# Kernel optimization log

Hardware: AMD Instinct MI355X
Metric: run time of the kernel (lower is better)

## Reference

```python
import jax, jax.numpy as jnp
import numpy as np

B, NQ, NKV, D, H = 2, 2048, 2048, 1024, 16
DH = D // H
EPS = 1e-5


def _ln(x, g, b):
    mu = jnp.mean(x, axis=-1, keepdims=True)
    var = jnp.mean(jnp.square(x - mu), axis=-1, keepdims=True)
    return (x - mu) * jax.lax.rsqrt(var + EPS) * g + b


def setup_inputs() -> dict:
    key = jax.random.key(0)
    ks = jax.random.split(key, 16)
    s = 0.02
    return {
        "X": jax.random.normal(ks[0], (B, NQ, D), jnp.float32),
        "Y": jax.random.normal(ks[1], (B, NKV, D), jnp.float32),
        "Wq": jax.random.normal(ks[2], (D, D), jnp.float32) * s,
        "bq": jnp.zeros((D,), jnp.float32),
        "Wk": jax.random.normal(ks[3], (D, D), jnp.float32) * s,
        "bk": jnp.zeros((D,), jnp.float32),
        "Wv": jax.random.normal(ks[4], (D, D), jnp.float32) * s,
        "bv": jnp.zeros((D,), jnp.float32),
        "null_k": jax.random.normal(ks[5], (1, 1, D), jnp.float32) * s,
        "g0": jnp.ones((D,), jnp.float32),
        "b0": jnp.zeros((D,), jnp.float32),
        "g0kv": jnp.ones((D,), jnp.float32),
        "b0kv": jnp.zeros((D,), jnp.float32),
        "g1": jnp.ones((D,), jnp.float32),
        "b1": jnp.zeros((D,), jnp.float32),
        "W1": jax.random.normal(ks[6], (D, 4 * D), jnp.float32) * s,
        "bf1": jnp.zeros((4 * D,), jnp.float32),
        "W2": jax.random.normal(ks[7], (4 * D, D), jnp.float32) * s,
        "bf2": jnp.zeros((D,), jnp.float32),
    }


def reference(X, Y, Wq, bq, Wk, bk, Wv, bv, null_k, g0, b0, g0kv, b0kv,
              g1, b1, W1, bf1, W2, bf2):
    # pre-layer-norm on Q-side and KV-side inputs
    Xn = _ln(X, g0, b0)
    Yn = _ln(Y, g0kv, b0kv)
    Q = Xn @ Wq + bq                       # [B, NQ, D]
    K = Yn @ Wk + bk                       # [B, NKV, D]
    V = Yn @ Wv + bv
    # null KV: learned null key, zero value appended along seq dim
    K = jnp.concatenate([K, jnp.broadcast_to(null_k, (B, 1, D))], axis=1)   # [B, NKV+1, D]
    V = jnp.concatenate([V, jnp.zeros((B, 1, D), V.dtype)], axis=1)
    # split heads (split along feature dim == reshape to (.., H, DH))
    Qh = Q.reshape(B, NQ, H, DH)
    Kh = K.reshape(B, NKV + 1, H, DH)
    Vh = V.reshape(B, NKV + 1, H, DH)
    # scores scaled by 1/sqrt(dim_KV) (NOT head dim), softmax_temp == 1.0
    A = jnp.einsum('bqhd,bkhd->bhqk', Qh, Kh) / jnp.sqrt(jnp.float32(D))
    A = jax.nn.softmax(A, axis=-1)          # [B, H, NQ, NKV+1]
    O = jnp.einsum('bhqk,bkhd->bqhd', A, Vh).reshape(B, NQ, D)
    # no head mixing (fc_mix_heads=None); residual uses identity fc_res
    Hres = O + X
    Hr = _ln(Hres, g1, b1)
    ff = jax.nn.gelu(Hr @ W1 + bf1, approximate=False) @ W2 + bf2
    return Hres + ff
```

## Files before the change

kernel.cpp:

```cpp
#include <hip/hip_runtime.h>
#include <hip/hip_bf16.h>
#include <math.h>
#include <stdint.h>

typedef __bf16 bf16x8 __attribute__((ext_vector_type(8)));
typedef __bf16 bf16x4 __attribute__((ext_vector_type(4)));
typedef float floatx4 __attribute__((ext_vector_type(4)));
typedef short shortx4 __attribute__((ext_vector_type(4)));

#define NQS   2048
#define NKVS  2048
#define NKV1  2049
#define DM    1024
#define NH    16
#define DHD   64
#define BATCH 2
#define ROWS  (BATCH * NQS)

__device__ __forceinline__ void gld_lds16(const __bf16* gp, __bf16* lp) {
    __builtin_amdgcn_global_load_lds(
        (const __attribute__((address_space(1))) uint32_t*)(uintptr_t)gp,
        (__attribute__((address_space(3))) uint32_t*)(uintptr_t)lp,
        16, 0, 0);
}

__device__ __forceinline__ float gelu_fast(float x) {
    const float u = x * x;
    const float e = __builtin_amdgcn_exp2f(x * (-2.3022077f + (-0.1029431f) * u));
    return x * __builtin_amdgcn_rcpf(1.0f + e);
}

__global__ __launch_bounds__(256) void ln2_to_bf16(
    const float* __restrict__ X, const float* __restrict__ Y,
    const float* __restrict__ g0, const float* __restrict__ b0,
    const float* __restrict__ g0kv, const float* __restrict__ b0kv,
    __bf16* __restrict__ Xn, __bf16* __restrict__ Yn)
{
    int row = blockIdx.x;
    const float *src, *gamma, *beta; __bf16* dst;
    if (row < ROWS) { src = X; gamma = g0; beta = b0; dst = Xn; }
    else { row -= ROWS; src = Y; gamma = g0kv; beta = b0kv; dst = Yn; }
    const int tid = threadIdx.x;
    const float4 v = ((const float4*)(src + (size_t)row * DM))[tid];
    float s  = v.x + v.y + v.z + v.w;
    float sq = v.x * v.x + v.y * v.y + v.z * v.z + v.w * v.w;
    for (int off = 1; off < 64; off <<= 1) {
        s  += __shfl_xor(s, off);
        sq += __shfl_xor(sq, off);
    }
    __shared__ float red[8];
    const int wave = tid >> 6, lane = tid & 63;
    if (lane == 0) { red[wave * 2] = s; red[wave * 2 + 1] = sq; }
    __syncthreads();
    s  = red[0] + red[2] + red[4] + red[6];
    sq = red[1] + red[3] + red[5] + red[7];
    const float mu  = s * (1.0f / DM);
    const float var = sq * (1.0f / DM) - mu * mu;
    const float rs  = rsqrtf(var + 1e-5f);
    const float4 gv = ((const float4*)gamma)[tid];
    const float4 bv = ((const float4*)beta)[tid];
    bf16x4 o;
    o[0] = (__bf16)((v.x - mu) * rs * gv.x + bv.x);
    o[1] = (__bf16)((v.y - mu) * rs * gv.y + bv.y);
    o[2] = (__bf16)((v.z - mu) * rs * gv.z + bv.z);
    o[3] = (__bf16)((v.w - mu) * rs * gv.w + bv.w);
    *(bf16x4*)(dst + (size_t)row * DM + tid * 4) = o;
}

__global__ __launch_bounds__(256) void resid_ln(
    const float* __restrict__ X, const __bf16* __restrict__ O,
    const float* __restrict__ gamma, const float* __restrict__ beta,
    float* __restrict__ Hres, __bf16* __restrict__ Hr)
{
    const int row = blockIdx.x;
    const int tid = threadIdx.x;
    const float4 xv = ((const float4*)(X + (size_t)row * DM))[tid];
    const bf16x4 ov = *(const bf16x4*)(O + (size_t)row * DM + tid * 4);
    float4 v;
    v.x = xv.x + (float)ov[0];
    v.y = xv.y + (float)ov[1];
    v.z = xv.z + (float)ov[2];
    v.w = xv.w + (float)ov[3];
    ((float4*)(Hres + (size_t)row * DM))[tid] = v;

    float s  = v.x + v.y + v.z + v.w;
    float sq = v.x * v.x + v.y * v.y + v.z * v.z + v.w * v.w;
    for (int off = 1; off < 64; off <<= 1) {
        s  += __shfl_xor(s, off);
        sq += __shfl_xor(sq, off);
    }
    __shared__ float red[8];
    const int wave = tid >> 6, lane = tid & 63;
    if (lane == 0) { red[wave * 2] = s; red[wave * 2 + 1] = sq; }
    __syncthreads();
    s  = red[0] + red[2] + red[4] + red[6];
    sq = red[1] + red[3] + red[5] + red[7];
    const float mu  = s * (1.0f / DM);
    const float var = sq * (1.0f / DM) - mu * mu;
    const float rs  = rsqrtf(var + 1e-5f);
    const float4 gv = ((const float4*)gamma)[tid];
    const float4 bv = ((const float4*)beta)[tid];
    bf16x4 o;
    o[0] = (__bf16)((v.x - mu) * rs * gv.x + bv.x);
    o[1] = (__bf16)((v.y - mu) * rs * gv.y + bv.y);
    o[2] = (__bf16)((v.z - mu) * rs * gv.z + bv.z);
    o[3] = (__bf16)((v.w - mu) * rs * gv.w + bv.w);
    *(bf16x4*)(Hr + (size_t)row * DM + tid * 4) = o;
}

__global__ __launch_bounds__(256) void transpose3_f32_bf16(
    const float* __restrict__ Wq, const float* __restrict__ Wk,
    const float* __restrict__ Wv, __bf16* __restrict__ WqT,
    __bf16* __restrict__ WkT, __bf16* __restrict__ WvT)
{
    __shared__ float tile[32][33];
    const int z = blockIdx.z;
    const float* in = (z == 0) ? Wq : (z == 1) ? Wk : Wv;
    __bf16* out = (z == 0) ? WqT : (z == 1) ? WkT : WvT;
    const int c0 = blockIdx.x * 32, r0 = blockIdx.y * 32;
    const int tx = threadIdx.x, ty = threadIdx.y;
#pragma unroll
    for (int i = 0; i < 4; i++)
        tile[ty + i * 8][tx] = in[(size_t)(r0 + ty + i * 8) * DM + c0 + tx];
    __syncthreads();
#pragma unroll
    for (int i = 0; i < 4; i++)
        out[(size_t)(c0 + ty + i * 8) * DM + r0 + tx] = (__bf16)tile[tx][ty + i * 8];
}

__global__ __launch_bounds__(256) void transpose_ffw(
    const float* __restrict__ W1, const float* __restrict__ W2,
    __bf16* __restrict__ W1T, __bf16* __restrict__ W2T)
{
    __shared__ float tile[32][33];
    const int z = blockIdx.z;
    const float* in; __bf16* out; int R, C, c0, r0;
    if (z == 0) { in = W1; out = W1T; R = DM; C = 4 * DM; c0 = blockIdx.x * 32; r0 = blockIdx.y * 32; }
    else        { in = W2; out = W2T; R = 4 * DM; C = DM; c0 = blockIdx.y * 32; r0 = blockIdx.x * 32; }
    const int tx = threadIdx.x, ty = threadIdx.y;
#pragma unroll
    for (int i = 0; i < 4; i++)
        tile[ty + i * 8][tx] = in[(size_t)(r0 + ty + i * 8) * C + c0 + tx];
    __syncthreads();
#pragma unroll
    for (int i = 0; i < 4; i++)
        out[(size_t)(c0 + ty + i * 8) * R + r0 + tx] = (__bf16)tile[tx][ty + i * 8];
}

__global__ __launch_bounds__(256) void fill_null(
    const float* __restrict__ null_k, __bf16* __restrict__ Kb,
    __bf16* __restrict__ Vt)
{
    const int i = blockIdx.x * 256 + threadIdx.x;
    if (i < BATCH * DM) {
        const int b = i >> 10, d = i & (DM - 1);
        Kb[((size_t)b * NKV1 + NKVS) * DM + d] = (__bf16)null_k[d];
    }
    if (i < BATCH * NH * DHD * 8) {
        const int bhd = i >> 3, kvp = i & 7;
        Vt[(size_t)bhd * 2056 + 2048 + kvp] = (__bf16)0.0f;
    }
}

__device__ __forceinline__ void g256_loop(
    const __bf16* __restrict__ A, const __bf16* __restrict__ Bt,
    int Kst, int kbeg, int m0, int n0,
    __bf16* sa, __bf16* sb, floatx4 (&acc)[8][4])
{
    const int tid = threadIdx.x, lane = tid & 63;
    const int g = lane >> 4, c = lane & 15;
    const int wave = tid >> 6;
    const int wm = wave >> 2, wn = wave & 3;

    const int r = tid >> 2, j = tid & 3;
    const int jx = (j ^ (r & 3)) * 8;
    const __bf16* Ag = A  + (size_t)(m0 + r) * Kst + kbeg + jx;
    const __bf16* Bg = Bt + (size_t)(n0 + r) * Kst + kbeg + jx;
    __bf16* la = sa + tid * 8;
    __bf16* lb = sb + tid * 8;

#define G256_STAGE(ss, koff) do {                                          \
    gld_lds16(Ag + (koff),                      la + (ss) * 8192);         \
    gld_lds16(Ag + (size_t)128 * Kst + (koff),  la + (ss) * 8192 + 4096);  \
    gld_lds16(Bg + (koff),                      lb + (ss) * 8192);         \
    gld_lds16(Bg + (size_t)128 * Kst + (koff),  lb + (ss) * 8192 + 4096);  \
} while (0)

    G256_STAGE(0, 0);
    G256_STAGE(1, 32);
    G256_STAGE(2, 64);

    const int ca = (c & 3) * 8;
    const __bf16* ra = sa + (wm * 128 + c) * 32;
    const __bf16* rb = sb + (wn * 64 + c) * 32;

    for (int s = 0; s < 32; s++) {
        if (s < 29) {
            G256_STAGE((s + 3) & 3, (s + 3) * 32);
            asm volatile("s_waitcnt vmcnt(12)" ::: "memory");
        } else if (s == 29) {
            asm volatile("s_waitcnt vmcnt(8)" ::: "memory");
        } else if (s == 30) {
            asm volatile("s_waitcnt vmcnt(4)" ::: "memory");
        } else {
            asm volatile("s_waitcnt vmcnt(0)" ::: "memory");
        }
        __builtin_amdgcn_sched_barrier(0);
        __builtin_amdgcn_s_barrier();
        asm volatile("" ::: "memory");

        const int ss = (s & 3) * 8192;
        bf16x8 af[8], bfr[4];
#pragma unroll
        for (int i = 0; i < 8; i++)
            af[i] = *(const bf16x8*)(ra + ss + i * 512 + ((g * 8) ^ ca));
#pragma unroll
        for (int jj = 0; jj < 4; jj++)
            bfr[jj] = *(const bf16x8*)(rb + ss + jj * 512 + ((g * 8) ^ ca));

        __builtin_amdgcn_s_setprio(1);
#pragma unroll
        for (int i = 0; i < 8; i++)
#pragma unroll
            for (int jj = 0; jj < 4; jj++)
                acc[i][jj] = __builtin_amdgcn_mfma_f32_16x16x32_bf16(
                    af[i], bfr[jj], acc[i][jj], 0, 0, 0);
        __builtin_amdgcn_s_setprio(0);
        __builtin_amdgcn_sched_barrier(0);
        __builtin_amdgcn_s_barrier();
        asm volatile("" ::: "memory");
    }
#undef G256_STAGE
}

template<int NX>
__device__ __forceinline__ void g256_decode(int bid, int ntot, int& m0, int& n0)
{
    const int cpx = ntot >> 3;
    const int l = (bid & 7) * cpx + (bid >> 3);
    m0 = (l / NX) * 256;
    n0 = (l % NX) * 256;
}

template<int MODE, int ACT, int NX>
__global__ __launch_bounds__(512, 2) void g256(
    const __bf16* __restrict__ A, const __bf16* __restrict__ Bt,
    const float* __restrict__ bias, void* __restrict__ outp,
    int M, int N, int Kst)
{
    __shared__ __bf16 SA[4][256][32];
    __shared__ __bf16 SB[4][256][32];
    int m0, n0;
    g256_decode<NX>(blockIdx.x, NX * (M >> 8), m0, n0);
    const int kbeg = (MODE == 4) ? (blockIdx.z << 10) : 0;

    floatx4 acc[8][4] = {};
    g256_loop(A, Bt, Kst, kbeg, m0, n0, &SA[0][0][0], &SB[0][0][0], acc);

    const int tid = threadIdx.x, lane = tid & 63, wave = tid >> 6;
    const int g = lane >> 4, c = lane & 15;
    const int wm = wave >> 2, wn = wave & 3;

    __bf16* obf = (__bf16*)outp;
    float*  of  = (float*)outp;
#pragma unroll
    for (int i = 0; i < 8; i++) {
#pragma unroll
        for (int jj = 0; jj < 4; jj++) {
            const int row = m0 + wm * 128 + i * 16 + g * 4;
            const int col = n0 + wn * 64 + jj * 16 + c;
            const float bb = (MODE == 4) ? 0.0f : bias[col];
            float xs[4];
#pragma unroll
            for (int rr = 0; rr < 4; rr++) {
                float x = acc[i][jj][rr] + bb;
                if (ACT == 1) x = gelu_fast(x);
                xs[rr] = x;
            }
            if (MODE == 0) {
#pragma unroll
                for (int rr = 0; rr < 4; rr++)
                    obf[(size_t)(row + rr) * N + col] = (__bf16)xs[rr];
            } else if (MODE == 4) {
#pragma unroll
                for (int rr = 0; rr < 4; rr++)
                    of[((size_t)blockIdx.z * M + row + rr) * N + col] = xs[rr];
            }
        }
    }
}

__global__ __launch_bounds__(512, 2) void g256qkv(
    const __bf16* __restrict__ Xn, const __bf16* __restrict__ Yn,
    const __bf16* __restrict__ WqT, const __bf16* __restrict__ WkT,
    const __bf16* __restrict__ WvT,
    const float* __restrict__ bq, const float* __restrict__ bk,
    const float* __restrict__ bv,
    __bf16* __restrict__ Qbf, __bf16* __restrict__ Kbf,
    __bf16* __restrict__ Vt)
{
    __shared__ __bf16 SA[4][256][32];
    __shared__ __bf16 SB[4][256][32];
    const int z = blockIdx.z;
    const __bf16* A    = (z == 0) ? Xn  : Yn;
    const __bf16* Bt   = (z == 0) ? WqT : (z == 1) ? WkT : WvT;
    const float*  bias = (z == 0) ? bq  : (z == 1) ? bk  : bv;

    int m0, n0;
    g256_decode<4>(blockIdx.x, 64, m0, n0);

    floatx4 acc[8][4] = {};
    g256_loop(A, Bt, DM, 0, m0, n0, &SA[0][0][0], &SB[0][0][0], acc);

    const int tid = threadIdx.x, lane = tid & 63, wave = tid >> 6;
    const int g = lane >> 4, c = lane & 15;
    const int wm = wave >> 2, wn = wave & 3;

#pragma unroll
    for (int i = 0; i < 8; i++) {
#pragma unroll
        for (int jj = 0; jj < 4; jj++) {
            const int row = m0 + wm * 128 + i * 16 + g * 4;
            const int col = n0 + wn * 64 + jj * 16 + c;
            const float bb = bias[col];
            float xs[4];
#pragma unroll
            for (int rr = 0; rr < 4; rr++) xs[rr] = acc[i][jj][rr] + bb;
            if (z == 0) {
#pragma unroll
                for (int rr = 0; rr < 4; rr++)
                    Qbf[(size_t)(row + rr) * DM + col] = (__bf16)xs[rr];
            } else if (z == 1) {
#pragma unroll
                for (int rr = 0; rr < 4; rr++) {
                    const int r2 = row + rr;
                    Kbf[(size_t)(r2 + (r2 >> 11)) * DM + col] = (__bf16)xs[rr];
                }
            } else {
                const int b  = row >> 11;
                const int kv = row & 2047;
                const size_t base =
                    ((size_t)((b * NH + (col >> 6)) * DHD + (col & 63))) * 2056 + kv;
                bf16x4 pk;
                pk[0] = (__bf16)xs[0]; pk[1] = (__bf16)xs[1];
                pk[2] = (__bf16)xs[2]; pk[3] = (__bf16)xs[3];
                *(bf16x4*)(Vt + base) = pk;
            }
        }
    }
}

__global__ __launch_bounds__(256) void ff2_reduce(
    const float* __restrict__ part, const float* __restrict__ bias,
    const float* __restrict__ Hres, float* __restrict__ out)
{
    const size_t f4 = (size_t)blockIdx.x * 256 + threadIdx.x;
    const int c4 = (int)(f4 & (DM / 4 - 1));
    const size_t stride4 = (size_t)ROWS * DM / 4;
    float4 a = ((const float4*)part)[f4];
    const float4 p1 = ((const float4*)part)[f4 + stride4];
    const float4 p2 = ((const float4*)part)[f4 + 2 * stride4];
    const float4 p3 = ((const float4*)part)[f4 + 3 * stride4];
    const float4 b  = ((const float4*)bias)[c4];
    const float4 hr = ((const float4*)Hres)[f4];
    a.x += p1.x + p2.x + p3.x + b.x + hr.x;
    a.y += p1.y + p2.y + p3.y + b.y + hr.y;
    a.z += p1.z + p2.z + p3.z + b.z + hr.z;
    a.w += p1.w + p2.w + p3.w + b.w + hr.w;
    ((float4*)out)[f4] = a;
}

__global__ __launch_bounds__(256, 2) void attn_kernel(
    const __bf16* __restrict__ Q, const __bf16* __restrict__ Kb,
    const __bf16* __restrict__ Vt, __bf16* __restrict__ O)
{
    __shared__ __bf16 Ks[4][64][64];
    __shared__ __bf16 Vs[4][64][64];

    const int tid = threadIdx.x, lane = tid & 63, w = tid >> 6;
    const int g = lane >> 4, c = lane & 15;

    const int hw   = blockIdx.x;
    const int slot = hw >> 3;
    const int hb   = (hw & 7) | ((slot >> 4) << 3);
    const int h = hb & 15, b = hb >> 4;
    const int q0w = (slot & 15) * 128 + w * 32;

    const float QSC = 0.03125f * 1.44269504088896f;
    bf16x8 qf[2][2];
#pragma unroll
    for (int qt = 0; qt < 2; qt++) {
        const __bf16* Qbase = Q + ((size_t)(b * NQS + q0w + qt * 16 + c)) * DM + h * DHD;
        qf[qt][0] = *(const bf16x8*)(Qbase + g * 8);
        qf[qt][1] = *(const bf16x8*)(Qbase + 32 + g * 8);
#pragma unroll
        for (int e = 0; e < 8; e++) {
            qf[qt][0][e] = (__bf16)((float)qf[qt][0][e] * QSC);
            qf[qt][1][e] = (__bf16)((float)qf[qt][1][e] * QSC);
        }
    }

    shortx4 ones;
    ones[0] = ones[1] = ones[2] = ones[3] = (short)0x3F80;

    floatx4 dacc[2] = {};
    floatx4 oacc[2][4] = {};

    const int srow = tid >> 3;
    const int schk = (tid & 7) ^ (srow & 7);
    const __bf16* Kg  = Kb + (size_t)b * NKV1 * DM + h * DHD + schk * 8;
    const __bf16* Vg  = Vt + ((size_t)(b * NH + h) * DHD + srow) * 2056;
    const __bf16* Vg2 = Vg + (size_t)32 * 2056;
    const int vcol0 = schk * 8;

    auto stage = [&](int p, int kv0, bool tail) {
        __bf16* kd0 = &Ks[p][0][0]  + tid * 8;
        __bf16* kd1 = &Ks[p][32][0] + tid * 8;
        __bf16* vd0 = &Vs[p][0][0]  + tid * 8;
        __bf16* vd1 = &Vs[p][32][0] + tid * 8;
        if (!tail) {
            gld_lds16(Kg + (size_t)(kv0 + srow) * DM, kd0);
            gld_lds16(Kg + (size_t)(kv0 + srow + 32) * DM, kd1);
            gld_lds16(Vg + kv0 + vcol0, vd0);
            gld_lds16(Vg2 + kv0 + vcol0, vd1);
        } else {
            const int r0 = min(kv0 + srow, NKVS);
            const int r1 = min(kv0 + srow + 32, NKVS);
            const int vc = min(kv0 + vcol0, NKVS);
            gld_lds16(Kg + (size_t)r0 * DM, kd0);
            gld_lds16(Kg + (size_t)r1 * DM, kd1);
            gld_lds16(Vg + vc, vd0);
            gld_lds16(Vg2 + vc, vd1);
        }
    };

    auto compute = [&](int p, int kv0, bool tail) {
        floatx4 s[2][4];
#pragma unroll
        for (int qt = 0; qt < 2; qt++)
#pragma unroll
            for (int kvt = 0; kvt < 4; kvt++)
#pragma unroll
                for (int r = 0; r < 4; r++) s[qt][kvt][r] = -6.0f;

        const int sw = c & 7;
        __builtin_amdgcn_s_setprio(1);
#pragma unroll
        for (int kvt = 0; kvt < 4; kvt++) {
            const bf16x8 kf0 = *(const bf16x8*)&Ks[p][kvt * 16 + c][(g ^ sw) * 8];
            const bf16x8 kf1 = *(const bf16x8*)&Ks[p][kvt * 16 + c][((4 | g) ^ sw) * 8];
#pragma unroll
            for (int qt = 0; qt < 2; qt++) {
                s[qt][kvt] = __builtin_amdgcn_mfma_f32_16x16x32_bf16(kf0, qf[qt][0], s[qt][kvt], 0, 0, 0);
                s[qt][kvt] = __builtin_amdgcn_mfma_f32_16x16x32_bf16(kf1, qf[qt][1], s[qt][kvt], 0, 0, 0);
            }
        }
        __builtin_amdgcn_s_setprio(0);

        if (tail) {
#pragma unroll
            for (int qt = 0; qt < 2; qt++)
#pragma unroll
                for (int kvt = 0; kvt < 4; kvt++)
#pragma unroll
                    for (int r = 0; r < 4; r++)
                        if (kv0 + kvt * 16 + g * 4 + r >= NKV1) s[qt][kvt][r] = -1e30f;
        }

        shortx4 pf[2][4];
#pragma unroll
        for (int qt = 0; qt < 2; qt++)
#pragma unroll
            for (int kvt = 0; kvt < 4; kvt++) {
                const unsigned u0 = __builtin_bit_cast(unsigned, __builtin_amdgcn_exp2f(s[qt][kvt][0]));
                const unsigned u1 = __builtin_bit_cast(unsigned, __builtin_amdgcn_exp2f(s[qt][kvt][1]));
                const unsigned u2 = __builtin_bit_cast(unsigned, __builtin_amdgcn_exp2f(s[qt][kvt][2]));
                const unsigned u3 = __builtin_bit_cast(unsigned, __builtin_amdgcn_exp2f(s[qt][kvt][3]));
                unsigned pk0 = __builtin_amdgcn_perm(u1, u0, 0x07060302u);
                unsigned pk1 = __builtin_amdgcn_perm(u3, u2, 0x07060302u);
                unsigned long long pk = ((unsigned long long)pk1 << 32) | pk0;
                pf[qt][kvt] = __builtin_bit_cast(shortx4, pk);
            }

        __builtin_amdgcn_s_setprio(1);
#pragma unroll
        for (int kvt = 0; kvt < 4; kvt++) {
            shortx4 vfr[4];
#pragma unroll
            for (int dt = 0; dt < 4; dt++) {
                const int slotp = (kvt * 2 + (g >> 1)) ^ sw;
                vfr[dt] = *(const shortx4*)&Vs[p][dt * 16 + c][slotp * 8 + (g & 1) * 4];
            }
#pragma unroll
            for (int dt = 0; dt < 4; dt++)
#pragma unroll
                for (int qt = 0; qt < 2; qt++)
                    oacc[qt][dt] = __builtin_amdgcn_mfma_f32_16x16x16bf16_1k(
                        vfr[dt], pf[qt][kvt], oacc[qt][dt], 0, 0, 0);
#pragma unroll
            for (int qt = 0; qt < 2; qt++)
                dacc[qt] = __builtin_amdgcn_mfma_f32_16x16x16bf16_1k(
                    ones, pf[qt][kvt], dacc[qt], 0, 0, 0);
        }
        __builtin_amdgcn_s_setprio(0);
    };

    stage(0, 0, false);
    stage(1, 64, false);
    __syncthreads();
    for (int it = 0; it < 32; it += 2) {
        stage((it + 2) & 3, (it + 2) * 64, (it + 2) == 32);
        if (it + 3 <= 32) stage((it + 3) & 3, (it + 3) * 64, false);
        compute(it & 3, it * 64, false);
        compute((it + 1) & 3, (it + 1) * 64, false);
        __syncthreads();
    }
    compute(0, 2048, true);

#pragma unroll
    for (int qt = 0; qt < 2; qt++) {
        const float inv_l = 1.0f / dacc[qt][0];
        __bf16* Ob = O + ((size_t)(b * NQS + q0w + qt * 16 + c)) * DM + h * DHD;
#pragma unroll
        for (int dt = 0; dt < 4; dt++) {
            bf16x4 ob;
#pragma unroll
            for (int r = 0; r < 4; r++) ob[r] = (__bf16)(oacc[qt][dt][r] * inv_l);
            *(bf16x4*)(Ob + dt * 16 + g * 4) = ob;
        }
    }
}

extern "C" void kernel_launch(void* const* d_in, const int* in_sizes, int n_in,
                              void* d_out, int out_size, void* d_ws, size_t ws_size,
                              hipStream_t stream)
{
    const float* X      = (const float*)d_in[0];
    const float* Y      = (const float*)d_in[1];
    const float* Wq     = (const float*)d_in[2];
    const float* bq     = (const float*)d_in[3];
    const float* Wk     = (const float*)d_in[4];
    const float* bk     = (const float*)d_in[5];
    const float* Wv     = (const float*)d_in[6];
    const float* bv     = (const float*)d_in[7];
    const float* null_k = (const float*)d_in[8];
    const float* g0     = (const float*)d_in[9];
    const float* b0     = (const float*)d_in[10];
    const float* g0kv   = (const float*)d_in[11];
    const float* b0kv   = (const float*)d_in[12];
    const float* g1     = (const float*)d_in[13];
    const float* b1     = (const float*)d_in[14];
    const float* W1     = (const float*)d_in[15];
    const float* bf1    = (const float*)d_in[16];
    const float* W2     = (const float*)d_in[17];
    const float* bf2    = (const float*)d_in[18];
    float* out = (float*)d_out;

    char* p = (char*)d_ws;
    __bf16* W2T  = (__bf16*)p; p += (size_t)4 * DM * DM * 2;
    float*  Hres = (float*)p;  p += (size_t)ROWS * DM * 4;
    __bf16* Gbf  = (__bf16*)p; p += (size_t)ROWS * 4 * DM * 2;
    char* scratch = p;
    __bf16* Xn   = (__bf16*)p; p += (size_t)ROWS * DM * 2;
    __bf16* Yn   = (__bf16*)p; p += (size_t)ROWS * DM * 2;
    __bf16* WqT  = (__bf16*)p; p += (size_t)DM * DM * 2;
    __bf16* WkT  = (__bf16*)p; p += (size_t)DM * DM * 2;
    __bf16* WvT  = (__bf16*)p; p += (size_t)DM * DM * 2;
    __bf16* W1T  = (__bf16*)p; p += (size_t)4 * DM * DM * 2;
    __bf16* Qbf  = (__bf16*)p; p += (size_t)ROWS * DM * 2;
    __bf16* Kbf  = (__bf16*)p; p += (size_t)BATCH * NKV1 * DM * 2;
    __bf16* Vt   = (__bf16*)p; p += (size_t)BATCH * NH * DHD * 2056 * 2;
    __bf16* Obf  = (__bf16*)p; p += (size_t)ROWS * DM * 2;
    __bf16* Hr   = (__bf16*)p; p += (size_t)ROWS * DM * 2;
    float* Part  = (float*)scratch;

    ln2_to_bf16<<<2 * ROWS, 256, 0, stream>>>(X, Y, g0, b0, g0kv, b0kv, Xn, Yn);

    transpose3_f32_bf16<<<dim3(DM / 32, DM / 32, 3), dim3(32, 8), 0, stream>>>(
        Wq, Wk, Wv, WqT, WkT, WvT);
    transpose_ffw<<<dim3(128, 32, 2), dim3(32, 8), 0, stream>>>(W1, W2, W1T, W2T);

    g256qkv<<<dim3(64, 1, 3), 512, 0, stream>>>(
        Xn, Yn, WqT, WkT, WvT, bq, bk, bv, Qbf, Kbf, Vt);
    fill_null<<<64, 256, 0, stream>>>(null_k, Kbf, Vt);

    attn_kernel<<<dim3(512), 256, 0, stream>>>(Qbf, Kbf, Vt, Obf);

    resid_ln<<<ROWS, 256, 0, stream>>>(X, Obf, g1, b1, Hres, Hr);

    g256<0, 1, 16><<<dim3(256), 512, 0, stream>>>(
        Hr, W1T, bf1, (void*)Gbf, ROWS, 4 * DM, DM);
    g256<4, 0, 4><<<dim3(64, 1, 4), 512, 0, stream>>>(
        Gbf, W2T, bf2, (void*)Part, ROWS, DM, 4 * DM);
    ff2_reduce<<<ROWS * DM / 1024, 256, 0, stream>>>(Part, bf2, Hres, out);
}
```

Before: 353.0 us.

## Interleave LDS reads, global prefetch and MFMA in four phases per k-step

Restructures the 256x256 GEMM main loop so each k-step is split into four phases. Each phase loads two A fragments from LDS, issues one of the four global-to-LDS prefetch loads, synchronizes, and runs eight MFMAs. The vmcnt wait is relaxed to match the spread-out issue. The intent is to overlap LDS reads and global loads with MFMA work and lower register pressure by holding only two A fragments at a time. It also lowers launch bounds from two to one block per CU, which frees registers but may cut occupancy, and adds three extra barriers per k-step.

```diff
diff --git a/kernel.cpp b/kernel.cpp
--- a/kernel.cpp
+++ b/kernel.cpp
@@ -193,42 +193,89 @@
     const int ca = (c & 3) * 8;
     const __bf16* ra = sa + (wm * 128 + c) * 32;
     const __bf16* rb = sb + (wn * 64 + c) * 32;
+    const int rx = (g * 8) ^ ca;
 
     for (int s = 0; s < 32; s++) {
-        if (s < 29) {
-            G256_STAGE((s + 3) & 3, (s + 3) * 32);
-            asm volatile("s_waitcnt vmcnt(12)" ::: "memory");
-        } else if (s == 29) {
-            asm volatile("s_waitcnt vmcnt(8)" ::: "memory");
-        } else if (s == 30) {
-            asm volatile("s_waitcnt vmcnt(4)" ::: "memory");
-        } else {
-            asm volatile("s_waitcnt vmcnt(0)" ::: "memory");
-        }
+        if (s <= 29)      asm volatile("s_waitcnt vmcnt(8)" ::: "memory");
+        else if (s == 30) asm volatile("s_waitcnt vmcnt(4)" ::: "memory");
+        else              asm volatile("s_waitcnt vmcnt(0)" ::: "memory");
         __builtin_amdgcn_sched_barrier(0);
         __builtin_amdgcn_s_barrier();
         asm volatile("" ::: "memory");
 
         const int ss = (s & 3) * 8192;
-        bf16x8 af[8], bfr[4];
-#pragma unroll
-        for (int i = 0; i < 8; i++)
-            af[i] = *(const bf16x8*)(ra + ss + i * 512 + ((g * 8) ^ ca));
-#pragma unroll
-        for (int jj = 0; jj < 4; jj++)
-            bfr[jj] = *(const bf16x8*)(rb + ss + jj * 512 + ((g * 8) ^ ca));
-
+        const bool st = (s < 29);
+        const int s3 = (s + 3) & 3;
+        const int k3 = (s + 3) * 32;
+        bf16x8 bfr[4], a0, a1;
+
+        bfr[0] = *(const bf16x8*)(rb + ss + 0 * 512 + rx);
+        bfr[1] = *(const bf16x8*)(rb + ss + 1 * 512 + rx);
+        bfr[2] = *(const bf16x8*)(rb + ss + 2 * 512 + rx);
+        bfr[3] = *(const bf16x8*)(rb + ss + 3 * 512 + rx);
+        a0 = *(const bf16x8*)(ra + ss + 0 * 512 + rx);
+        a1 = *(const bf16x8*)(ra + ss + 1 * 512 + rx);
+        if (st) gld_lds16(Ag + k3, la + s3 * 8192);
+        __builtin_amdgcn_sched_barrier(0);
+        __builtin_amdgcn_s_barrier();
+        asm volatile("s_waitcnt lgkmcnt(0)" ::: "memory");
+        __builtin_amdgcn_sched_barrier(0);
         __builtin_amdgcn_s_setprio(1);
 #pragma unroll
-        for (int i = 0; i < 8; i++)
-#pragma unroll
-            for (int jj = 0; jj < 4; jj++)
-                acc[i][jj] = __builtin_amdgcn_mfma_f32_16x16x32_bf16(
-                    af[i], bfr[jj], acc[i][jj], 0, 0, 0);
+        for (int jj = 0; jj < 4; jj++) {
+            acc[0][jj] = __builtin_amdgcn_mfma_f32_16x16x32_bf16(a0, bfr[jj], acc[0][jj], 0, 0, 0);
+            acc[1][jj] = __builtin_amdgcn_mfma_f32_16x16x32_bf16(a1, bfr[jj], acc[1][jj], 0, 0, 0);
+        }
         __builtin_amdgcn_s_setprio(0);
         __builtin_amdgcn_sched_barrier(0);
+
+        a0 = *(const bf16x8*)(ra + ss + 2 * 512 + rx);
+        a1 = *(const bf16x8*)(ra + ss + 3 * 512 + rx);
+        if (st) gld_lds16(Ag + (size_t)128 * Kst + k3, la + s3 * 8192 + 4096);
+        __builtin_amdgcn_sched_barrier(0);
         __builtin_amdgcn_s_barrier();
-        asm volatile("" ::: "memory");
+        asm volatile("s_waitcnt lgkmcnt(0)" ::: "memory");
+        __builtin_amdgcn_sched_barrier(0);
+        __builtin_amdgcn_s_setprio(1);
+#pragma unroll
+        for (int jj = 0; jj < 4; jj++) {
+            acc[2][jj] = __builtin_amdgcn_mfma_f32_16x16x32_bf16(a0, bfr[jj], acc[2][jj], 0, 0, 0);
+            acc[3][jj] = __builtin_amdgcn_mfma_f32_16x16x32_bf16(a1, bfr[jj], acc[3][jj], 0, 0, 0);
+        }
+        __builtin_amdgcn_s_setprio(0);
+        __builtin_amdgcn_sched_barrier(0);
+
+        a0 = *(const bf16x8*)(ra + ss + 4 * 512 + rx);
+        a1 = *(const bf16x8*)(ra + ss + 5 * 512 + rx);
+        if (st) gld_lds16(Bg + k3, lb + s3 * 8192);
+        __builtin_amdgcn_sched_barrier(0);
+        __builtin_amdgcn_s_barrier();
+        asm volatile("s_waitcnt lgkmcnt(0)" ::: "memory");
+        __builtin_amdgcn_sched_barrier(0);
+        __builtin_amdgcn_s_setprio(1);
+#pragma unroll
+        for (int jj = 0; jj < 4; jj++) {
+            acc[4][jj] = __builtin_amdgcn_mfma_f32_16x16x32_bf16(a0, bfr[jj], acc[4][jj], 0, 0, 0);
+            acc[5][jj] = __builtin_amdgcn_mfma_f32_16x16x32_bf16(a1, bfr[jj], acc[5][jj], 0, 0, 0);
+        }
+        __builtin_amdgcn_s_setprio(0);
+        __builtin_amdgcn_sched_barrier(0);
+
+        a0 = *(const bf16x8*)(ra + ss + 6 * 512 + rx);
+        a1 = *(const bf16x8*)(ra + ss + 7 * 512 + rx);
+        if (st) gld_lds16(Bg + (size_t)128 * Kst + k3, lb + s3 * 8192 + 4096);
+        __builtin_amdgcn_sched_barrier(0);
+        __builtin_amdgcn_s_barrier();
+        asm volatile("s_waitcnt lgkmcnt(0)" ::: "memory");
+        __builtin_amdgcn_sched_barrier(0);
+        __builtin_amdgcn_s_setprio(1);
+#pragma unroll
+        for (int jj = 0; jj < 4; jj++) {
+            acc[6][jj] = __builtin_amdgcn_mfma_f32_16x16x32_bf16(a0, bfr[jj], acc[6][jj], 0, 0, 0);
+            acc[7][jj] = __builtin_amdgcn_mfma_f32_16x16x32_bf16(a1, bfr[jj], acc[7][jj], 0, 0, 0);
+        }
+        __builtin_amdgcn_s_setprio(0);
+        __builtin_amdgcn_sched_barrier(0);
     }
 #undef G256_STAGE
 }
@@ -243,7 +290,7 @@
 }
 
 template<int MODE, int ACT, int NX>
-__global__ __launch_bounds__(512, 2) void g256(
+__global__ __launch_bounds__(512, 1) void g256(
     const __bf16* __restrict__ A, const __bf16* __restrict__ Bt,
     const float* __restrict__ bias, void* __restrict__ outp,
     int M, int N, int Kst)
@@ -290,7 +337,7 @@
     }
 }
 
-__global__ __launch_bounds__(512, 2) void g256qkv(
+__global__ __launch_bounds__(512, 1) void g256qkv(
     const __bf16* __restrict__ Xn, const __bf16* __restrict__ Yn,
     const __bf16* __restrict__ WqT, const __bf16* __restrict__ WkT,
     const __bf16* __restrict__ WvT,
```

Result: faster. 342.0 us (-3.1%).

## Shrink GEMM tiles to 128x128 with 256-thread blocks and double buffering

Applied to the files above, without the earlier changes.

Replaces the 256x256 GEMM tile (512 threads, 4-stage LDS pipeline) with a 128x128 tile (256 threads, 2-stage pipeline) for the QKV, FF1 and FF2 GEMMs. Grid sizes grow four-fold, which gives the 256 CUs more blocks and better load balance, and lets more blocks fit per CU. In exchange each tile reuses its loaded data less, so global traffic per FLOP goes up, and the shallower prefetch exposes more memory latency.

```diff
diff --git a/kernel.cpp b/kernel.cpp
--- a/kernel.cpp
+++ b/kernel.cpp
@@ -162,15 +162,15 @@
     }
 }
 
-__device__ __forceinline__ void g256_loop(
+__device__ __forceinline__ void g128_loop(
     const __bf16* __restrict__ A, const __bf16* __restrict__ Bt,
-    int Kst, int kbeg, int m0, int n0,
-    __bf16* sa, __bf16* sb, floatx4 (&acc)[8][4])
+    int Kst, int kbeg, int ns, int m0, int n0,
+    __bf16* sa, __bf16* sb, floatx4 (&acc)[4][4])
 {
     const int tid = threadIdx.x, lane = tid & 63;
     const int g = lane >> 4, c = lane & 15;
     const int wave = tid >> 6;
-    const int wm = wave >> 2, wn = wave & 3;
+    const int wm = (wave >> 1) * 64, wn = (wave & 1) * 64;
 
     const int r = tid >> 2, j = tid & 3;
     const int jx = (j ^ (r & 3)) * 8;
@@ -179,28 +179,22 @@
     __bf16* la = sa + tid * 8;
     __bf16* lb = sb + tid * 8;
 
-#define G256_STAGE(ss, koff) do {                                          \
-    gld_lds16(Ag + (koff),                      la + (ss) * 8192);         \
-    gld_lds16(Ag + (size_t)128 * Kst + (koff),  la + (ss) * 8192 + 4096);  \
-    gld_lds16(Bg + (koff),                      lb + (ss) * 8192);         \
-    gld_lds16(Bg + (size_t)128 * Kst + (koff),  lb + (ss) * 8192 + 4096);  \
+#define G128_STAGE(ss, koff) do {                                         \
+    gld_lds16(Ag + (koff),                     la + (ss) * 4096);         \
+    gld_lds16(Ag + (size_t)64 * Kst + (koff),  la + (ss) * 4096 + 2048);  \
+    gld_lds16(Bg + (koff),                     lb + (ss) * 4096);         \
+    gld_lds16(Bg + (size_t)64 * Kst + (koff),  lb + (ss) * 4096 + 2048);  \
 } while (0)
 
-    G256_STAGE(0, 0);
-    G256_STAGE(1, 32);
-    G256_STAGE(2, 64);
-
-    const int ca = (c & 3) * 8;
-    const __bf16* ra = sa + (wm * 128 + c) * 32;
-    const __bf16* rb = sb + (wn * 64 + c) * 32;
-
-    for (int s = 0; s < 32; s++) {
-        if (s < 29) {
-            G256_STAGE((s + 3) & 3, (s + 3) * 32);
-            asm volatile("s_waitcnt vmcnt(12)" ::: "memory");
-        } else if (s == 29) {
-            asm volatile("s_waitcnt vmcnt(8)" ::: "memory");
-        } else if (s == 30) {
+    G128_STAGE(0, 0);
+
+    const int rx = (g * 8) ^ ((c & 3) * 8);
+    const __bf16* ra = sa + (wm + c) * 32;
+    const __bf16* rb = sb + (wn + c) * 32;
+
+    for (int s = 0; s < ns; s++) {
+        if (s + 1 < ns) {
+            G128_STAGE((s + 1) & 1, (s + 1) * 32);
             asm volatile("s_waitcnt vmcnt(4)" ::: "memory");
         } else {
             asm volatile("s_waitcnt vmcnt(0)" ::: "memory");
@@ -209,18 +203,18 @@
         __builtin_amdgcn_s_barrier();
         asm volatile("" ::: "memory");
 
-        const int ss = (s & 3) * 8192;
-        bf16x8 af[8], bfr[4];
-#pragma unroll
-        for (int i = 0; i < 8; i++)
-            af[i] = *(const bf16x8*)(ra + ss + i * 512 + ((g * 8) ^ ca));
+        const int ss = (s & 1) * 4096;
+        bf16x8 af[4], bfr[4];
+#pragma unroll
+        for (int i = 0; i < 4; i++)
+            af[i] = *(const bf16x8*)(ra + ss + i * 512 + rx);
 #pragma unroll
         for (int jj = 0; jj < 4; jj++)
-            bfr[jj] = *(const bf16x8*)(rb + ss + jj * 512 + ((g * 8) ^ ca));
+            bfr[jj] = *(const bf16x8*)(rb + ss + jj * 512 + rx);
 
         __builtin_amdgcn_s_setprio(1);
 #pragma unroll
-        for (int i = 0; i < 8; i++)
+        for (int i = 0; i < 4; i++)
 #pragma unroll
             for (int jj = 0; jj < 4; jj++)
                 acc[i][jj] = __builtin_amdgcn_mfma_f32_16x16x32_bf16(
@@ -230,45 +224,46 @@
         __builtin_amdgcn_s_barrier();
         asm volatile("" ::: "memory");
     }
-#undef G256_STAGE
+#undef G128_STAGE
 }
 
 template<int NX>
-__device__ __forceinline__ void g256_decode(int bid, int ntot, int& m0, int& n0)
+__device__ __forceinline__ void g128_decode(int bid, int ntot, int& m0, int& n0)
 {
     const int cpx = ntot >> 3;
     const int l = (bid & 7) * cpx + (bid >> 3);
-    m0 = (l / NX) * 256;
-    n0 = (l % NX) * 256;
+    m0 = (l / NX) * 128;
+    n0 = (l % NX) * 128;
 }
 
 template<int MODE, int ACT, int NX>
-__global__ __launch_bounds__(512, 2) void g256(
+__global__ __launch_bounds__(256, 4) void g128(
     const __bf16* __restrict__ A, const __bf16* __restrict__ Bt,
     const float* __restrict__ bias, void* __restrict__ outp,
-    int M, int N, int Kst)
-{
-    __shared__ __bf16 SA[4][256][32];
-    __shared__ __bf16 SB[4][256][32];
+    int M, int N, int K)
+{
+    __shared__ __bf16 SA[2][128][32];
+    __shared__ __bf16 SB[2][128][32];
     int m0, n0;
-    g256_decode<NX>(blockIdx.x, NX * (M >> 8), m0, n0);
-    const int kbeg = (MODE == 4) ? (blockIdx.z << 10) : 0;
-
-    floatx4 acc[8][4] = {};
-    g256_loop(A, Bt, Kst, kbeg, m0, n0, &SA[0][0][0], &SB[0][0][0], acc);
+    g128_decode<NX>(blockIdx.x, NX * (M >> 7), m0, n0);
+    const int kbeg = (MODE == 4) ? blockIdx.z * (K >> 2) : 0;
+    const int ns = ((MODE == 4) ? (K >> 2) : K) >> 5;
+
+    floatx4 acc[4][4] = {};
+    g128_loop(A, Bt, K, kbeg, ns, m0, n0, &SA[0][0][0], &SB[0][0][0], acc);
 
     const int tid = threadIdx.x, lane = tid & 63, wave = tid >> 6;
     const int g = lane >> 4, c = lane & 15;
-    const int wm = wave >> 2, wn = wave & 3;
+    const int wm = (wave >> 1) * 64, wn = (wave & 1) * 64;
 
     __bf16* obf = (__bf16*)outp;
     float*  of  = (float*)outp;
 #pragma unroll
-    for (int i = 0; i < 8; i++) {
+    for (int i = 0; i < 4; i++) {
 #pragma unroll
         for (int jj = 0; jj < 4; jj++) {
-            const int row = m0 + wm * 128 + i * 16 + g * 4;
-            const int col = n0 + wn * 64 + jj * 16 + c;
+            const int row = m0 + wm + i * 16 + g * 4;
+            const int col = n0 + wn + jj * 16 + c;
             const float bb = (MODE == 4) ? 0.0f : bias[col];
             float xs[4];
 #pragma unroll
@@ -290,7 +285,7 @@
     }
 }
 
-__global__ __launch_bounds__(512, 2) void g256qkv(
+__global__ __launch_bounds__(256, 4) void g128qkv(
     const __bf16* __restrict__ Xn, const __bf16* __restrict__ Yn,
     const __bf16* __restrict__ WqT, const __bf16* __restrict__ WkT,
     const __bf16* __restrict__ WvT,
@@ -299,29 +294,29 @@
     __bf16* __restrict__ Qbf, __bf16* __restrict__ Kbf,
     __bf16* __restrict__ Vt)
 {
-    __shared__ __bf16 SA[4][256][32];
-    __shared__ __bf16 SB[4][256][32];
+    __shared__ __bf16 SA[2][128][32];
+    __shared__ __bf16 SB[2][128][32];
     const int z = blockIdx.z;
     const __bf16* A    = (z == 0) ? Xn  : Yn;
     const __bf16* Bt   = (z == 0) ? WqT : (z == 1) ? WkT : WvT;
     const float*  bias = (z == 0) ? bq  : (z == 1) ? bk  : bv;
 
     int m0, n0;
-    g256_decode<4>(blockIdx.x, 64, m0, n0);
-
-    floatx4 acc[8][4] = {};
-    g256_loop(A, Bt, DM, 0, m0, n0, &SA[0][0][0], &SB[0][0][0], acc);
+    g128_decode<8>(blockIdx.x, 256, m0, n0);
+
+    floatx4 acc[4][4] = {};
+    g128_loop(A, Bt, DM, 0, DM >> 5, m0, n0, &SA[0][0][0], &SB[0][0][0], acc);
 
     const int tid = threadIdx.x, lane = tid & 63, wave = tid >> 6;
     const int g = lane >> 4, c = lane & 15;
-    const int wm = wave >> 2, wn = wave & 3;
-
-#pragma unroll
-    for (int i = 0; i < 8; i++) {
+    const int wm = (wave >> 1) * 64, wn = (wave & 1) * 64;
+
+#pragma unroll
+    for (int i = 0; i < 4; i++) {
 #pragma unroll
         for (int jj = 0; jj < 4; jj++) {
-            const int row = m0 + wm * 128 + i * 16 + g * 4;
-            const int col = n0 + wn * 64 + jj * 16 + c;
+            const int row = m0 + wm + i * 16 + g * 4;
+            const int col = n0 + wn + jj * 16 + c;
             const float bb = bias[col];
             float xs[4];
 #pragma unroll
@@ -580,7 +575,7 @@
         Wq, Wk, Wv, WqT, WkT, WvT);
     transpose_ffw<<<dim3(128, 32, 2), dim3(32, 8), 0, stream>>>(W1, W2, W1T, W2T);
 
-    g256qkv<<<dim3(64, 1, 3), 512, 0, stream>>>(
+    g128qkv<<<dim3(256, 1, 3), 256, 0, stream>>>(
         Xn, Yn, WqT, WkT, WvT, bq, bk, bv, Qbf, Kbf, Vt);
     fill_null<<<64, 256, 0, stream>>>(null_k, Kbf, Vt);
 
@@ -588,9 +583,9 @@
 
     resid_ln<<<ROWS, 256, 0, stream>>>(X, Obf, g1, b1, Hres, Hr);
 
-    g256<0, 1, 16><<<dim3(256), 512, 0, stream>>>(
+    g128<0, 1, 32><<<1024, 256, 0, stream>>>(
         Hr, W1T, bf1, (void*)Gbf, ROWS, 4 * DM, DM);
-    g256<4, 0, 4><<<dim3(64, 1, 4), 512, 0, stream>>>(
+    g128<4, 0, 8><<<dim3(256, 1, 4), 256, 0, stream>>>(
         Gbf, W2T, bf2, (void*)Part, ROWS, DM, 4 * DM);
     ff2_reduce<<<ROWS * DM / 1024, 256, 0, stream>>>(Part, bf2, Hres, out);
 }
```

Result: no change. 353.6 us (+0.2%).

## Restructure 256x256 GEMM mainloop to double-buffered K=64 tiles with interleaved loads

Applied to the files above, without the earlier changes.

The GEMM mainloop switches from a 4-stage K=32 LDS ring to a 2-stage K=64 double buffer. The next tile's global-to-LDS loads are split across four compute sub-phases so they overlap with MFMA work. A new XOR swizzle is used for the wider rows. LDS grows to 128KB per block, so launch bounds drop to one block per CU. The aim is fewer barriers per K and better load/compute interleaving, at the cost of occupancy and extra intra-tile barriers.

```diff
diff --git a/kernel.cpp b/kernel.cpp
--- a/kernel.cpp
+++ b/kernel.cpp
@@ -164,7 +164,7 @@
 
 __device__ __forceinline__ void g256_loop(
     const __bf16* __restrict__ A, const __bf16* __restrict__ Bt,
-    int Kst, int kbeg, int m0, int n0,
+    int Kst, int kbeg, int nt, int m0, int n0,
     __bf16* sa, __bf16* sb, floatx4 (&acc)[8][4])
 {
     const int tid = threadIdx.x, lane = tid & 63;
@@ -172,65 +172,90 @@
     const int wave = tid >> 6;
     const int wm = wave >> 2, wn = wave & 3;
 
-    const int r = tid >> 2, j = tid & 3;
-    const int jx = (j ^ (r & 3)) * 8;
-    const __bf16* Ag = A  + (size_t)(m0 + r) * Kst + kbeg + jx;
-    const __bf16* Bg = Bt + (size_t)(n0 + r) * Kst + kbeg + jx;
+    const int srow = tid >> 3;
+    const int jsrc = ((tid & 7) ^ (((tid >> 5) & 1) << 1)) * 8;
+    const __bf16* Ag = A  + (size_t)(m0 + srow) * Kst + kbeg + jsrc;
+    const __bf16* Bg = Bt + (size_t)(n0 + srow) * Kst + kbeg + jsrc;
     __bf16* la = sa + tid * 8;
     __bf16* lb = sb + tid * 8;
 
-#define G256_STAGE(ss, koff) do {                                          \
-    gld_lds16(Ag + (koff),                      la + (ss) * 8192);         \
-    gld_lds16(Ag + (size_t)128 * Kst + (koff),  la + (ss) * 8192 + 4096);  \
-    gld_lds16(Bg + (koff),                      lb + (ss) * 8192);         \
-    gld_lds16(Bg + (size_t)128 * Kst + (koff),  lb + (ss) * 8192 + 4096);  \
+#define STG_A(d, hf, kt) do {                                                   \
+    gld_lds16(Ag + (size_t)((hf) * 128) * Kst + (kt) * 64,                      \
+              la + (d) * 16384 + (hf) * 8192);                                  \
+    gld_lds16(Ag + (size_t)((hf) * 128 + 64) * Kst + (kt) * 64,                 \
+              la + (d) * 16384 + (hf) * 8192 + 4096);                           \
 } while (0)
-
-    G256_STAGE(0, 0);
-    G256_STAGE(1, 32);
-    G256_STAGE(2, 64);
-
-    const int ca = (c & 3) * 8;
-    const __bf16* ra = sa + (wm * 128 + c) * 32;
-    const __bf16* rb = sb + (wn * 64 + c) * 32;
-
-    for (int s = 0; s < 32; s++) {
-        if (s < 29) {
-            G256_STAGE((s + 3) & 3, (s + 3) * 32);
-            asm volatile("s_waitcnt vmcnt(12)" ::: "memory");
-        } else if (s == 29) {
-            asm volatile("s_waitcnt vmcnt(8)" ::: "memory");
-        } else if (s == 30) {
-            asm volatile("s_waitcnt vmcnt(4)" ::: "memory");
-        } else {
-            asm volatile("s_waitcnt vmcnt(0)" ::: "memory");
-        }
+#define STG_B(d, hf, kt) do {                                                   \
+    gld_lds16(Bg + (size_t)((hf) * 128) * Kst + (kt) * 64,                      \
+              lb + (d) * 16384 + (hf) * 8192);                                  \
+    gld_lds16(Bg + (size_t)((hf) * 128 + 64) * Kst + (kt) * 64,                 \
+              lb + (d) * 16384 + (hf) * 8192 + 4096);                           \
+} while (0)
+
+    STG_A(0, 0, 0); STG_A(0, 1, 0); STG_B(0, 0, 0); STG_B(0, 1, 0);
+
+    const int flip2 = ((c >> 2) & 1) << 1;
+    const __bf16* ra = sa + (wm * 128 + c) * 64;
+    const __bf16* rb = sb + (wn * 64 + c) * 64;
+
+    for (int t = 0; t < nt; t++) {
+        const int d = t & 1, dn = d ^ 1;
+        const bool more = (t + 1 < nt);
+        if (more) STG_A(dn, 0, t + 1);
+        if (more) asm volatile("s_waitcnt vmcnt(2)" ::: "memory");
+        else      asm volatile("s_waitcnt vmcnt(0)" ::: "memory");
         __builtin_amdgcn_sched_barrier(0);
         __builtin_amdgcn_s_barrier();
         asm volatile("" ::: "memory");
 
-        const int ss = (s & 3) * 8192;
-        bf16x8 af[8], bfr[4];
-#pragma unroll
-        for (int i = 0; i < 8; i++)
-            af[i] = *(const bf16x8*)(ra + ss + i * 512 + ((g * 8) ^ ca));
-#pragma unroll
-        for (int jj = 0; jj < 4; jj++)
-            bfr[jj] = *(const bf16x8*)(rb + ss + jj * 512 + ((g * 8) ^ ca));
-
-        __builtin_amdgcn_s_setprio(1);
-#pragma unroll
-        for (int i = 0; i < 8; i++)
-#pragma unroll
-            for (int jj = 0; jj < 4; jj++)
-                acc[i][jj] = __builtin_amdgcn_mfma_f32_16x16x32_bf16(
-                    af[i], bfr[jj], acc[i][jj], 0, 0, 0);
-        __builtin_amdgcn_s_setprio(0);
-        __builtin_amdgcn_sched_barrier(0);
-        __builtin_amdgcn_s_barrier();
-        asm volatile("" ::: "memory");
-    }
-#undef G256_STAGE
+        const __bf16* rad = ra + d * 16384;
+        const __bf16* rbd = rb + d * 16384;
+        bf16x8 bfr[4][2];
+
+#pragma unroll
+        for (int q = 0; q < 4; q++) {
+            if (q == 0) {
+#pragma unroll
+                for (int n = 0; n < 4; n++)
+#pragma unroll
+                    for (int kk = 0; kk < 2; kk++)
+                        bfr[n][kk] = *(const bf16x8*)(
+                            rbd + n * 1024 + (((kk * 4 + g) ^ flip2) * 8));
+            }
+            bf16x8 af[2][2];
+#pragma unroll
+            for (int u = 0; u < 2; u++)
+#pragma unroll
+                for (int kk = 0; kk < 2; kk++)
+                    af[u][kk] = *(const bf16x8*)(
+                        rad + (q * 32 + u * 16) * 64 + (((kk * 4 + g) ^ flip2) * 8));
+            if (more) {
+                if (q == 0)      STG_A(dn, 1, t + 1);
+                else if (q == 1) STG_B(dn, 0, t + 1);
+                else if (q == 2) STG_B(dn, 1, t + 1);
+            }
+            if (q == 0) asm volatile("s_waitcnt lgkmcnt(8)" ::: "memory");
+            __builtin_amdgcn_sched_barrier(0);
+            __builtin_amdgcn_s_barrier();
+            asm volatile("s_waitcnt lgkmcnt(0)" ::: "memory");
+            __builtin_amdgcn_sched_barrier(0);
+            __builtin_amdgcn_s_setprio(1);
+#pragma unroll
+            for (int kk = 0; kk < 2; kk++)
+#pragma unroll
+                for (int u = 0; u < 2; u++)
+#pragma unroll
+                    for (int n = 0; n < 4; n++)
+                        acc[2 * q + u][n] = __builtin_amdgcn_mfma_f32_16x16x32_bf16(
+                            af[u][kk], bfr[n][kk], acc[2 * q + u][n], 0, 0, 0);
+            __builtin_amdgcn_s_setprio(0);
+            __builtin_amdgcn_sched_barrier(0);
+            __builtin_amdgcn_s_barrier();
+            asm volatile("" ::: "memory");
+        }
+    }
+#undef STG_A
+#undef STG_B
 }
 
 template<int NX>
@@ -243,19 +268,19 @@
 }
 
 template<int MODE, int ACT, int NX>
-__global__ __launch_bounds__(512, 2) void g256(
+__global__ __launch_bounds__(512, 1) void g256(
     const __bf16* __restrict__ A, const __bf16* __restrict__ Bt,
     const float* __restrict__ bias, void* __restrict__ outp,
     int M, int N, int Kst)
 {
-    __shared__ __bf16 SA[4][256][32];
-    __shared__ __bf16 SB[4][256][32];
+    __shared__ __bf16 SA[2][256][64];
+    __shared__ __bf16 SB[2][256][64];
     int m0, n0;
     g256_decode<NX>(blockIdx.x, NX * (M >> 8), m0, n0);
     const int kbeg = (MODE == 4) ? (blockIdx.z << 10) : 0;
 
     floatx4 acc[8][4] = {};
-    g256_loop(A, Bt, Kst, kbeg, m0, n0, &SA[0][0][0], &SB[0][0][0], acc);
+    g256_loop(A, Bt, Kst, kbeg, 16, m0, n0, &SA[0][0][0], &SB[0][0][0], acc);
 
     const int tid = threadIdx.x, lane = tid & 63, wave = tid >> 6;
     const int g = lane >> 4, c = lane & 15;
@@ -290,7 +315,7 @@
     }
 }
 
-__global__ __launch_bounds__(512, 2) void g256qkv(
+__global__ __launch_bounds__(512, 1) void g256qkv(
     const __bf16* __restrict__ Xn, const __bf16* __restrict__ Yn,
     const __bf16* __restrict__ WqT, const __bf16* __restrict__ WkT,
     const __bf16* __restrict__ WvT,
@@ -299,8 +324,8 @@
     __bf16* __restrict__ Qbf, __bf16* __restrict__ Kbf,
     __bf16* __restrict__ Vt)
 {
-    __shared__ __bf16 SA[4][256][32];
-    __shared__ __bf16 SB[4][256][32];
+    __shared__ __bf16 SA[2][256][64];
+    __shared__ __bf16 SB[2][256][64];
     const int z = blockIdx.z;
     const __bf16* A    = (z == 0) ? Xn  : Yn;
     const __bf16* Bt   = (z == 0) ? WqT : (z == 1) ? WkT : WvT;
@@ -310,7 +335,7 @@
     g256_decode<4>(blockIdx.x, 64, m0, n0);
 
     floatx4 acc[8][4] = {};
-    g256_loop(A, Bt, DM, 0, m0, n0, &SA[0][0][0], &SB[0][0][0], acc);
+    g256_loop(A, Bt, DM, 0, 16, m0, n0, &SA[0][0][0], &SB[0][0][0], acc);
 
     const int tid = threadIdx.x, lane = tid & 63, wave = tid >> 6;
     const int g = lane >> 4, c = lane & 15;
```

After: 343.6 us. 2.7% less time.
